# Performance work log

Measured on AMD Instinct MI355X. Metric: run time of the kernel, lower is better.

## Reference

```python
import jax, jax.numpy as jnp
import numpy as np

EPS = 1e-8
NUM_ITERATIONS = 3


def layer_norm(x, g, b, eps=EPS):
    m = jnp.mean(x, axis=-1, keepdims=True)
    v = jnp.mean((x - m) ** 2, axis=-1, keepdims=True)
    return (x - m) * jax.lax.rsqrt(v + eps) * g + b


def gru_cell(x, h, w_ih, w_hh, b_ih, b_hh):
    # PyTorch GRUCell: gates ordered (r, z, n)
    gi = x @ w_ih.T + b_ih  # [B*S, 3D]
    gh = h @ w_hh.T + b_hh
    i_r, i_z, i_n = jnp.split(gi, 3, axis=-1)
    h_r, h_z, h_n = jnp.split(gh, 3, axis=-1)
    r = jax.nn.sigmoid(i_r + h_r)
    z = jax.nn.sigmoid(i_z + h_z)
    n = jnp.tanh(i_n + r * h_n)
    return (1.0 - z) * n + z * h


def setup_inputs() -> dict:
    key = jax.random.key(0)
    ks = jax.random.split(key, 12)
    B, N, D, S = 64, 1024, 512, 16
    s = 1.0 / np.sqrt(D)
    return {
        "inputs": jax.random.normal(ks[0], (B, N, D), jnp.float32),
        "noise": jax.random.normal(ks[1], (B, S, D), jnp.float32),
        "slot_mu": jax.random.normal(ks[2], (1, 1, D), jnp.float32),
        "slot_log_sigma": jnp.zeros((1, 1, D), jnp.float32),
        "ln_in_g": jnp.ones((D,), jnp.float32),
        "ln_in_b": jnp.zeros((D,), jnp.float32),
        "ln_slots_g": jnp.ones((D,), jnp.float32),
        "ln_slots_b": jnp.zeros((D,), jnp.float32),
        "ln_mlp_g": jnp.ones((D,), jnp.float32),
        "ln_mlp_b": jnp.zeros((D,), jnp.float32),
        "Wq": jax.random.normal(ks[3], (D, D), jnp.float32) * s,
        "Wk": jax.random.normal(ks[4], (D, D), jnp.float32) * s,
        "Wv": jax.random.normal(ks[5], (D, D), jnp.float32) * s,
        "gru_w_ih": jax.random.normal(ks[6], (3 * D, D), jnp.float32) * s,
        "gru_w_hh": jax.random.normal(ks[7], (3 * D, D), jnp.float32) * s,
        "gru_b_ih": jnp.zeros((3 * D,), jnp.float32),
        "gru_b_hh": jnp.zeros((3 * D,), jnp.float32),
        "mlp_w1": jax.random.normal(ks[8], (D, D), jnp.float32) * s,
        "mlp_b1": jnp.zeros((D,), jnp.float32),
        "mlp_w2": jax.random.normal(ks[9], (D, D), jnp.float32) * s,
        "mlp_b2": jnp.zeros((D,), jnp.float32),
    }


def reference(inputs, noise, slot_mu, slot_log_sigma,
              ln_in_g, ln_in_b, ln_slots_g, ln_slots_b, ln_mlp_g, ln_mlp_b,
              Wq, Wk, Wv, gru_w_ih, gru_w_hh, gru_b_ih, gru_b_hh,
              mlp_w1, mlp_b1, mlp_w2, mlp_b2):
    B, N, D = inputs.shape
    S = noise.shape[1]
    scale = D ** (-0.5)

    # slot init: mu + sigma * eps
    slots = slot_mu + jnp.exp(slot_log_sigma) * noise  # [B,S,D]

    x = layer_norm(inputs, ln_in_g, ln_in_b)
    k = x @ Wk.T  # [B,N,D]
    v = x @ Wv.T

    for _ in range(NUM_ITERATIONS):
        slots_prev = slots
        sn = layer_norm(slots, ln_slots_g, ln_slots_b)
        q = sn @ Wq.T  # [B,S,D]
        attn_logits = jnp.einsum("bnd,bmd->bnm", q, k) * scale  # [B,S,N]
        attn = jax.nn.softmax(attn_logits, axis=-1)
        attn = attn / (jnp.sum(attn, axis=1, keepdims=True) + EPS)  # column-normalize over slots
        updates = jnp.einsum("bnm,bmd->bnd", attn, v)  # [B,S,D]
        slots = gru_cell(updates.reshape(-1, D), slots_prev.reshape(-1, D),
                         gru_w_ih, gru_w_hh, gru_b_ih, gru_b_hh).reshape(B, S, D)
        h = jax.nn.relu(layer_norm(slots, ln_mlp_g, ln_mlp_b) @ mlp_w1.T + mlp_b1)
        slots = slots + h @ mlp_w2.T + mlp_b2

    # proj_to_hidden is Identity (slot_dim == hidden_size); forward_dtype=float32
    return slots
```

## Files before the change

kernel.cpp:

```cpp
#include <hip/hip_runtime.h>
#include <hip/hip_bf16.h>
#include <cstdint>
#include <cstddef>


typedef __bf16 bf16x8 __attribute__((ext_vector_type(8)));
typedef float f32x4 __attribute__((ext_vector_type(4)));

__device__ __forceinline__ float bf2f(unsigned int u) {
  union { unsigned int i; float f; } v; v.i = u << 16; return v.f;
}
__device__ __forceinline__ unsigned short f2bf(float x) {
  __hip_bfloat16 h = __float2bfloat16(x);
  unsigned short u;
  __builtin_memcpy(&u, &h, 2);
  return u;
}

#define GLD16(gp, lp)                                                       \
  __builtin_amdgcn_global_load_lds(                                         \
      (const __attribute__((address_space(1))) void*)(gp),                  \
      (__attribute__((address_space(3))) void*)(lp), 16, 0, 0)


__global__ void wprep_k(const float* __restrict__ w1, const float* __restrict__ w2,
                        const float* __restrict__ wih, const float* __restrict__ whh,
                        const float* __restrict__ bih, const float* __restrict__ bhh,
                        const float* __restrict__ mu, const float* __restrict__ ls,
                        const float* __restrict__ noise,
                        unsigned short* __restrict__ w1_bf, unsigned short* __restrict__ w2_bf,
                        unsigned short* __restrict__ wih_bf, unsigned short* __restrict__ wcat,
                        float* __restrict__ bcat, float* __restrict__ slots) {
  int blk = blockIdx.x, t = threadIdx.x;
  if (blk < 1024) {
    int i = blk * 256 + t; w1_bf[i] = f2bf(w1[i]);
  } else if (blk < 2048) {
    int i = (blk - 1024) * 256 + t; w2_bf[i] = f2bf(w2[i]);
  } else if (blk < 5120) {
    int i = (blk - 2048) * 256 + t; wih_bf[i] = f2bf(wih[i]);
  } else if (blk < 7168) {
    int i = (blk - 5120) * 256 + t;
    int j = i >> 9, d = i & 511;
    wcat[(size_t)j * 1024 + 512 + d] = f2bf(whh[(size_t)j * 512 + d]);
  } else if (blk < 8192) {
    int i = (blk - 7168) * 256 + t;
    int j = i >> 9, d = i & 511;
    wcat[(size_t)(1536 + j) * 1024 + 512 + d] = f2bf(whh[(size_t)(1024 + j) * 512 + d]);
  } else if (blk < 10240) {
    int i = (blk - 8192) * 256 + t;
    if (i < 262144) {
      int j = i >> 9, d = i & 511;
      wcat[(size_t)(1536 + j) * 1024 + d] = 0;
    } else {
      int k = i - 262144;
      int j = k >> 9, d = k & 511;
      wcat[(size_t)(1024 + j) * 1024 + 512 + d] = 0;
    }
  } else if (blk < 10248) {
    int j = (blk - 10240) * 256 + t;
    float v;
    if (j < 1024)      v = bih[j] + bhh[j];
    else if (j < 1536) v = bih[j];
    else               v = bhh[j - 512];
    bcat[j] = v;
  } else {
    int i = (blk - 10248) * 256 + t;
    int d = i & 511;
    slots[i] = mu[d] + expf(ls[d]) * noise[i];
  }
}

__global__ __launch_bounds__(256) void tcast3_k(const float* __restrict__ Wq,
                                                const float* __restrict__ Wk,
                                                const float* __restrict__ Wv,
                                                unsigned short* __restrict__ wqT,
                                                unsigned short* __restrict__ wkT,
                                                unsigned short* __restrict__ wvT) {
  __shared__ float tt[32][33];
  const float* in = blockIdx.z == 0 ? Wq : (blockIdx.z == 1 ? Wk : Wv);
  unsigned short* out = blockIdx.z == 0 ? wqT : (blockIdx.z == 1 ? wkT : wvT);
  int c0 = blockIdx.x << 5, r0 = blockIdx.y << 5;
  int tx = threadIdx.x & 31, ty = threadIdx.x >> 5;
  #pragma unroll
  for (int i = 0; i < 4; ++i)
    tt[ty + 8 * i][tx] = in[(size_t)(r0 + ty + 8 * i) * 512 + c0 + tx];
  __syncthreads();
  #pragma unroll
  for (int i = 0; i < 4; ++i)
    out[(size_t)(c0 + ty + 8 * i) * 512 + r0 + tx] = f2bf(tt[tx][ty + 8 * i]);
}


__global__ __launch_bounds__(256) void ln_rows_k(
    const float* __restrict__ in, const float* __restrict__ g, const float* __restrict__ b,
    unsigned short* __restrict__ out, int rows) {
  int w = threadIdx.x >> 6, lane = threadIdx.x & 63;
  int row = (blockIdx.x << 2) + w;
  if (row >= rows) return;
  const float4* rp = reinterpret_cast<const float4*>(in + (size_t)row * 512);
  float4 v0 = rp[lane], v1 = rp[lane + 64];
  float s = v0.x + v0.y + v0.z + v0.w + v1.x + v1.y + v1.z + v1.w;
  float q = v0.x*v0.x + v0.y*v0.y + v0.z*v0.z + v0.w*v0.w
          + v1.x*v1.x + v1.y*v1.y + v1.z*v1.z + v1.w*v1.w;
  #pragma unroll
  for (int o = 32; o > 0; o >>= 1) { s += __shfl_xor(s, o); q += __shfl_xor(q, o); }
  float m = s * (1.0f / 512.0f);
  float rstd = rsqrtf(q * (1.0f / 512.0f) - m * m + 1e-8f);
  const float4* gp = reinterpret_cast<const float4*>(g);
  const float4* bp = reinterpret_cast<const float4*>(b);
  float4 g0 = gp[lane], g1 = gp[lane + 64];
  float4 b0 = bp[lane], b1 = bp[lane + 64];
  ushort4 o0, o1;
  o0.x = f2bf((v0.x - m) * rstd * g0.x + b0.x);
  o0.y = f2bf((v0.y - m) * rstd * g0.y + b0.y);
  o0.z = f2bf((v0.z - m) * rstd * g0.z + b0.z);
  o0.w = f2bf((v0.w - m) * rstd * g0.w + b0.w);
  o1.x = f2bf((v1.x - m) * rstd * g1.x + b1.x);
  o1.y = f2bf((v1.y - m) * rstd * g1.y + b1.y);
  o1.z = f2bf((v1.z - m) * rstd * g1.z + b1.z);
  o1.w = f2bf((v1.w - m) * rstd * g1.w + b1.w);
  ushort4* op = reinterpret_cast<ushort4*>(out + (size_t)row * 512);
  op[lane] = o0; op[lane + 64] = o1;
}


__global__ __launch_bounds__(256) void xt_k(const unsigned short* __restrict__ x,
                                            unsigned short* __restrict__ xT) {
  __shared__ unsigned short t[64][68];
  int nt = blockIdx.x, et = blockIdx.y, b = blockIdx.z;
  int r = threadIdx.x >> 3, c8 = (threadIdx.x & 7) << 3;
  #pragma unroll
  for (int p = 0; p < 2; ++p) {
    int row = r + (p << 5);
    *reinterpret_cast<uint4*>(&t[row][c8]) = *reinterpret_cast<const uint4*>(
        x + ((size_t)(b << 10) + (nt << 6) + row) * 512 + (et << 6) + c8);
  }
  __syncthreads();
  #pragma unroll
  for (int p = 0; p < 2; ++p) {
    int erow = r + (p << 5);
    ushort4 a, bb;
    #pragma unroll
    for (int j = 0; j < 4; ++j) ((unsigned short*)&a)[j] = t[c8 + j][erow];
    #pragma unroll
    for (int j = 0; j < 4; ++j) ((unsigned short*)&bb)[j] = t[c8 + 4 + j][erow];
    unsigned short* o = xT + ((size_t)(b << 9) + (et << 6) + erow) * 1024 + (nt << 6) + c8;
    *reinterpret_cast<ushort4*>(o) = a;
    *reinterpret_cast<ushort4*>(o + 4) = bb;
  }
}

__global__ __launch_bounds__(256) void gru_ln_k(
    const float* __restrict__ gates, const float* __restrict__ hp,
    const float* __restrict__ g, const float* __restrict__ b,
    float* __restrict__ sgru, unsigned short* __restrict__ lnm) {
  int w = threadIdx.x >> 6, lane = threadIdx.x & 63;
  int row = (blockIdx.x << 2) + w;
  size_t gb = (size_t)row * 2048 + (lane << 3);
  size_t hb = (size_t)row * 512 + (lane << 3);
  float rs[8], zs[8], in_[8], hn[8], hv[8], y[8];
  #pragma unroll
  for (int c = 0; c < 2; ++c) {
    *reinterpret_cast<float4*>(rs + 4*c)  = *reinterpret_cast<const float4*>(gates + gb + 4*c);
    *reinterpret_cast<float4*>(zs + 4*c)  = *reinterpret_cast<const float4*>(gates + gb + 512 + 4*c);
    *reinterpret_cast<float4*>(in_ + 4*c) = *reinterpret_cast<const float4*>(gates + gb + 1024 + 4*c);
    *reinterpret_cast<float4*>(hn + 4*c)  = *reinterpret_cast<const float4*>(gates + gb + 1536 + 4*c);
    *reinterpret_cast<float4*>(hv + 4*c)  = *reinterpret_cast<const float4*>(hp + hb + 4*c);
  }
  float s = 0.f, q = 0.f;
  #pragma unroll
  for (int j = 0; j < 8; ++j) {
    float r = 1.0f / (1.0f + expf(-rs[j]));
    float z = 1.0f / (1.0f + expf(-zs[j]));
    float n = tanhf(in_[j] + r * hn[j]);
    float h = (1.0f - z) * n + z * hv[j];
    y[j] = h; s += h; q += h * h;
  }
  #pragma unroll
  for (int o = 32; o > 0; o >>= 1) { s += __shfl_xor(s, o); q += __shfl_xor(q, o); }
  float m = s * (1.0f / 512.0f);
  float rstd = rsqrtf(q * (1.0f / 512.0f) - m * m + 1e-8f);
  const float* gg = g + (lane << 3);
  const float* bb = b + (lane << 3);
  #pragma unroll
  for (int c = 0; c < 2; ++c)
    *reinterpret_cast<float4*>(sgru + hb + 4*c) = *reinterpret_cast<const float4*>(y + 4*c);
  uint4 o4;
  unsigned int p[8];
  #pragma unroll
  for (int j = 0; j < 8; ++j) p[j] = f2bf((y[j] - m) * rstd * gg[j] + bb[j]);
  o4.x = p[0] | (p[1] << 16); o4.y = p[2] | (p[3] << 16);
  o4.z = p[4] | (p[5] << 16); o4.w = p[6] | (p[7] << 16);
  *reinterpret_cast<uint4*>(lnm + hb) = o4;
}


__global__ __launch_bounds__(256) void gemm_cat(
    const unsigned short* __restrict__ A, const unsigned short* __restrict__ W,
    unsigned short* __restrict__ Cout, int M, int N, int K, int ldc) {
  __shared__ unsigned short sA[2][8192];
  __shared__ unsigned short sB[2][8192];
  const int tid = threadIdx.x;
  const int lane = tid & 63, w = tid >> 6;

  int nwg = gridDim.x * gridDim.y;
  int flat = blockIdx.y * gridDim.x + blockIdx.x;
  if ((nwg & 7) == 0) { int c = nwg >> 3; flat = (flat & 7) * c + (flat >> 3); }
  const int row0 = (flat / gridDim.x) << 7;
  const int col0 = (flat % gridDim.x) << 7;

  const int wm = (w >> 1) << 6, wn = (w & 1) << 6;
  const int lrow = lane & 15, kt = (lane >> 4) << 3;
  const int sr8 = lane >> 3, sc8 = (lane & 7) << 3;

  f32x4 acc[4][4];
  #pragma unroll
  for (int m = 0; m < 4; ++m)
    #pragma unroll
    for (int n = 0; n < 4; ++n) acc[m][n] = f32x4{0.f, 0.f, 0.f, 0.f};

  auto stage = [&](int buf, int k0) {
    #pragma unroll
    for (int i = 0; i < 4; ++i) {
      int ii = (w << 2) + i;
      int r = (ii << 3) + sr8;
      GLD16(A + (size_t)(row0 + r) * K + k0 + sc8, &sA[buf][ii * 512]);
      GLD16(W + (size_t)(col0 + r) * K + k0 + sc8, &sB[buf][ii * 512]);
    }
  };

  stage(0, 0);
  const int nt = K >> 6;
  int cur = 0;
  for (int t = 0; t < nt; ++t) {
    __syncthreads();
    if (t + 1 < nt) stage(cur ^ 1, (t + 1) << 6);
    #pragma unroll
    for (int kk = 0; kk < 2; ++kk) {
      bf16x8 af[4], bfv[4];
      #pragma unroll
      for (int m = 0; m < 4; ++m)
        af[m] = *reinterpret_cast<const bf16x8*>(&sA[cur][(wm + m * 16 + lrow) * 64 + (kk << 5) + kt]);
      #pragma unroll
      for (int n = 0; n < 4; ++n)
        bfv[n] = *reinterpret_cast<const bf16x8*>(&sB[cur][(wn + n * 16 + lrow) * 64 + (kk << 5) + kt]);
      #pragma unroll
      for (int m = 0; m < 4; ++m)
        #pragma unroll
        for (int n = 0; n < 4; ++n)
          acc[m][n] = __builtin_amdgcn_mfma_f32_16x16x32_bf16(af[m], bfv[n], acc[m][n], 0, 0, 0);
    }
    cur ^= 1;
  }

  const int rb = (lane >> 4) << 2;
  #pragma unroll
  for (int m = 0; m < 4; ++m) {
    #pragma unroll
    for (int n = 0; n < 4; ++n) {
      int col = col0 + wn + n * 16 + lrow;
      #pragma unroll
      for (int r = 0; r < 4; ++r) {
        int row = row0 + wm + m * 16 + rb + r;
        Cout[(size_t)row * ldc + col] = f2bf(acc[m][n][r]);
      }
    }
  }
}


__global__ __launch_bounds__(256) void q2ln_k(
    const float* __restrict__ slots, const float* __restrict__ g, const float* __restrict__ b,
    const unsigned short* __restrict__ wpt, unsigned short* __restrict__ q2,
    unsigned short* __restrict__ A2) {
  __shared__ unsigned short s_sn[16 * 520];
  __shared__ unsigned short sB[2][8192];
  const int b_ = blockIdx.y, ct = blockIdx.x;
  const int lane = threadIdx.x & 63, w = threadIdx.x >> 6;
  const int lrow = lane & 15, kt = (lane >> 4) << 3;
  const int sr8 = lane >> 3, sc8 = (lane & 7) << 3;

  const float4* gp = reinterpret_cast<const float4*>(g);
  const float4* bp = reinterpret_cast<const float4*>(b);
  float4 g0 = gp[lane], g1 = gp[lane + 64];
  float4 b0 = bp[lane], b1 = bp[lane + 64];
  #pragma unroll
  for (int rr = 0; rr < 4; ++rr) {
    int r = w * 4 + rr;
    const float4* rp = reinterpret_cast<const float4*>(slots + (size_t)(b_ * 16 + r) * 512);
    float4 v0 = rp[lane], v1 = rp[lane + 64];
    float s = v0.x + v0.y + v0.z + v0.w + v1.x + v1.y + v1.z + v1.w;
    float q = v0.x*v0.x + v0.y*v0.y + v0.z*v0.z + v0.w*v0.w
            + v1.x*v1.x + v1.y*v1.y + v1.z*v1.z + v1.w*v1.w;
    #pragma unroll
    for (int o = 32; o > 0; o >>= 1) { s += __shfl_xor(s, o); q += __shfl_xor(q, o); }
    float m = s * (1.0f / 512.0f);
    float rstd = rsqrtf(q * (1.0f / 512.0f) - m * m + 1e-8f);
    ushort4 o0, o1;
    o0.x = f2bf((v0.x - m) * rstd * g0.x + b0.x);
    o0.y = f2bf((v0.y - m) * rstd * g0.y + b0.y);
    o0.z = f2bf((v0.z - m) * rstd * g0.z + b0.z);
    o0.w = f2bf((v0.w - m) * rstd * g0.w + b0.w);
    o1.x = f2bf((v1.x - m) * rstd * g1.x + b1.x);
    o1.y = f2bf((v1.y - m) * rstd * g1.y + b1.y);
    o1.z = f2bf((v1.z - m) * rstd * g1.z + b1.z);
    o1.w = f2bf((v1.w - m) * rstd * g1.w + b1.w);
    *reinterpret_cast<ushort4*>(&s_sn[r * 520 + lane * 4]) = o0;
    *reinterpret_cast<ushort4*>(&s_sn[r * 520 + 256 + lane * 4]) = o1;
    if (ct == 0) {
      ushort4 c0, c1;
      c0.x = f2bf(v0.x); c0.y = f2bf(v0.y); c0.z = f2bf(v0.z); c0.w = f2bf(v0.w);
      c1.x = f2bf(v1.x); c1.y = f2bf(v1.y); c1.z = f2bf(v1.z); c1.w = f2bf(v1.w);
      unsigned short* a2r = A2 + (size_t)(b_ * 16 + r) * 1024 + 512;
      *reinterpret_cast<ushort4*>(a2r + lane * 4) = c0;
      *reinterpret_cast<ushort4*>(a2r + 256 + lane * 4) = c1;
    }
  }

  const unsigned short* Bb = wpt + (size_t)(ct << 7) * 512;
  auto stage = [&](int buf, int k0) {
    #pragma unroll
    for (int i = 0; i < 4; ++i) {
      int ii = (w << 2) + i;
      GLD16(Bb + (size_t)((ii << 3) + sr8) * 512 + k0 + sc8, &sB[buf][ii * 512]);
    }
  };

  f32x4 acc[2];
  acc[0] = f32x4{0.f, 0.f, 0.f, 0.f};
  acc[1] = f32x4{0.f, 0.f, 0.f, 0.f};

  stage(0, 0);
  int cur = 0;
  for (int t = 0; t < 8; ++t) {
    __syncthreads();
    if (t + 1 < 8) stage(cur ^ 1, (t + 1) << 6);
    #pragma unroll
    for (int kk = 0; kk < 2; ++kk) {
      bf16x8 af = *reinterpret_cast<const bf16x8*>(&s_sn[lrow * 520 + (t << 6) + (kk << 5) + kt]);
      #pragma unroll
      for (int ni = 0; ni < 2; ++ni) {
        bf16x8 bfv = *reinterpret_cast<const bf16x8*>(
            &sB[cur][((w * 2 + ni) * 16 + lrow) * 64 + (kk << 5) + kt]);
        acc[ni] = __builtin_amdgcn_mfma_f32_16x16x32_bf16(af, bfv, acc[ni], 0, 0, 0);
      }
    }
    cur ^= 1;
  }

  const int rb = (lane >> 4) << 2;
  #pragma unroll
  for (int ni = 0; ni < 2; ++ni) {
    int col = (ct << 7) + (w * 2 + ni) * 16 + lrow;
    #pragma unroll
    for (int r = 0; r < 4; ++r) {
      int s = rb + r;
      q2[(size_t)((b_ << 4) + s) * 512 + col] = f2bf(acc[ni][r]);
    }
  }
}


__global__ __launch_bounds__(256) void logits_k(
    const unsigned short* __restrict__ q2, const unsigned short* __restrict__ x,
    unsigned short* __restrict__ out) {
  __shared__ unsigned short sA[2][1024];
  __shared__ unsigned short sB[2][8192];
  const int b = blockIdx.y, nt = blockIdx.x;
  const int lane = threadIdx.x & 63, w = threadIdx.x >> 6;
  const int lrow = lane & 15, kt = (lane >> 4) << 3;
  const int sr8 = lane >> 3, sc8 = (lane & 7) << 3;
  const unsigned short* Ab = q2 + ((size_t)b << 13);
  const unsigned short* Bb = x + (((size_t)(b << 10) + (nt << 7)) << 9);

  f32x4 acc[2];
  acc[0] = f32x4{0.f, 0.f, 0.f, 0.f};
  acc[1] = f32x4{0.f, 0.f, 0.f, 0.f};

  auto stage = [&](int buf, int k0) {
    #pragma unroll
    for (int i = 0; i < 4; ++i) {
      int ii = (w << 2) + i;
      GLD16(Bb + (size_t)((ii << 3) + sr8) * 512 + k0 + sc8, &sB[buf][ii * 512]);
    }
    if (w == 0) {
      #pragma unroll
      for (int i = 0; i < 2; ++i)
        GLD16(Ab + (size_t)((i << 3) + sr8) * 512 + k0 + sc8, &sA[buf][i * 512]);
    }
  };

  stage(0, 0);
  int cur = 0;
  for (int t = 0; t < 8; ++t) {
    __syncthreads();
    if (t + 1 < 8) stage(cur ^ 1, (t + 1) << 6);
    #pragma unroll
    for (int kk = 0; kk < 2; ++kk) {
      bf16x8 af = *reinterpret_cast<const bf16x8*>(&sA[cur][lrow * 64 + (kk << 5) + kt]);
      #pragma unroll
      for (int ni = 0; ni < 2; ++ni) {
        bf16x8 bfv = *reinterpret_cast<const bf16x8*>(
            &sB[cur][((w * 2 + ni) * 16 + lrow) * 64 + (kk << 5) + kt]);
        acc[ni] = __builtin_amdgcn_mfma_f32_16x16x32_bf16(af, bfv, acc[ni], 0, 0, 0);
      }
    }
    cur ^= 1;
  }

  const int rb = (lane >> 4) << 2;
  #pragma unroll
  for (int ni = 0; ni < 2; ++ni) {
    int n = (nt << 7) + (w * 2 + ni) * 16 + lrow;
    #pragma unroll
    for (int r = 0; r < 4; ++r) {
      int s = rb + r;
      out[(size_t)((b << 4) + s) * 1024 + n] = f2bf(acc[ni][r]);
    }
  }
}


__global__ __launch_bounds__(256) void pv_sm_k(
    const unsigned short* __restrict__ logits, const unsigned short* __restrict__ xT,
    unsigned short* __restrict__ A2) {
  __shared__ float s_mi[16][2];
  __shared__ unsigned short s_at[16 * 1032];
  __shared__ unsigned short sA[2][8192];
  const int b_ = blockIdx.y, et = blockIdx.x;
  const int lane = threadIdx.x & 63, w = threadIdx.x >> 6;
  const int lrow = lane & 15, kt = (lane >> 4) << 3;
  const int sr8 = lane >> 3, sc8 = (lane & 7) << 3;
  const unsigned short* lg = logits + ((size_t)b_ << 14);

  #pragma unroll
  for (int rr = 0; rr < 4; ++rr) {
    int r = w * 4 + rr;
    const unsigned short* rp = lg + (size_t)r * 1024;
    float v[16];
    float mx = -3.4e38f;
    #pragma unroll
    for (int i = 0; i < 16; ++i) { v[i] = bf2f(rp[lane + (i << 6)]); mx = fmaxf(mx, v[i]); }
    #pragma unroll
    for (int o = 32; o > 0; o >>= 1) mx = fmaxf(mx, __shfl_xor(mx, o));
    float s = 0.f;
    #pragma unroll
    for (int i = 0; i < 16; ++i) s += __expf(v[i] - mx);
    #pragma unroll
    for (int o = 32; o > 0; o >>= 1) s += __shfl_xor(s, o);
    if (lane == 0) { s_mi[r][0] = mx; s_mi[r][1] = 1.0f / s; }
  }
  __syncthreads();

  #pragma unroll
  for (int j = 0; j < 4; ++j) {
    int c = threadIdx.x + (j << 8);
    float e[16];
    float cs = 0.f;
    #pragma unroll
    for (int s = 0; s < 16; ++s) {
      e[s] = __expf(bf2f(lg[(size_t)s * 1024 + c]) - s_mi[s][0]) * s_mi[s][1];
      cs += e[s];
    }
    float rv = 1.0f / (cs + 1e-8f);
    #pragma unroll
    for (int s = 0; s < 16; ++s) s_at[s * 1032 + c] = f2bf(e[s] * rv);
  }

  const unsigned short* Ab = xT + ((size_t)b_ << 19) + (size_t)(et << 7) * 1024;
  auto stage = [&](int buf, int k0) {
    #pragma unroll
    for (int i = 0; i < 4; ++i) {
      int ii = (w << 2) + i;
      GLD16(Ab + (size_t)((ii << 3) + sr8) * 1024 + k0 + sc8, &sA[buf][ii * 512]);
    }
  };

  f32x4 acc[2];
  acc[0] = f32x4{0.f, 0.f, 0.f, 0.f};
  acc[1] = f32x4{0.f, 0.f, 0.f, 0.f};

  stage(0, 0);
  int cur = 0;
  for (int t = 0; t < 16; ++t) {
    __syncthreads();
    if (t + 1 < 16) stage(cur ^ 1, (t + 1) << 6);
    #pragma unroll
    for (int kk = 0; kk < 2; ++kk) {
      bf16x8 bfv = *reinterpret_cast<const bf16x8*>(&s_at[lrow * 1032 + (t << 6) + (kk << 5) + kt]);
      #pragma unroll
      for (int mi = 0; mi < 2; ++mi) {
        bf16x8 af = *reinterpret_cast<const bf16x8*>(
            &sA[cur][((w * 2 + mi) * 16 + lrow) * 64 + (kk << 5) + kt]);
        acc[mi] = __builtin_amdgcn_mfma_f32_16x16x32_bf16(af, bfv, acc[mi], 0, 0, 0);
      }
    }
    cur ^= 1;
  }

  const int rb = (lane >> 4) << 2;
  const int s = lrow;
  #pragma unroll
  for (int mi = 0; mi < 2; ++mi) {
    int e0 = (et << 7) + (w * 2 + mi) * 16 + rb;
    ushort4 o;
    o.x = f2bf(acc[mi][0]); o.y = f2bf(acc[mi][1]);
    o.z = f2bf(acc[mi][2]); o.w = f2bf(acc[mi][3]);
    *reinterpret_cast<ushort4*>(&A2[(size_t)((b_ << 4) + s) * 1024 + e0]) = o;
  }
}


template<int BIAS, int RELU, int ADDSRC, int OUTBF16, int SCALE>
__global__ __launch_bounds__(256) void gemm_sm(
    const unsigned short* __restrict__ A, const unsigned short* __restrict__ W,
    const float* __restrict__ bias, const float* __restrict__ addsrc,
    void* __restrict__ Cout, int M, int N, int K, float scalev) {
  __shared__ unsigned short sA[2][4096];
  __shared__ unsigned short sB[2][4096];
  const int tid = threadIdx.x;
  const int lane = tid & 63, w = tid >> 6;

  int nwg = gridDim.x * gridDim.y;
  int flat = blockIdx.y * gridDim.x + blockIdx.x;
  if ((nwg & 7) == 0) { int c = nwg >> 3; flat = (flat & 7) * c + (flat >> 3); }
  const int row0 = (flat / gridDim.x) << 6;
  const int col0 = (flat % gridDim.x) << 6;

  const int lrow = lane & 15, kt = (lane >> 4) << 3;
  const int sr8 = lane >> 3, sc8 = (lane & 7) << 3;

  f32x4 acc[4];
  #pragma unroll
  for (int m = 0; m < 4; ++m) acc[m] = f32x4{0.f, 0.f, 0.f, 0.f};

  auto stage = [&](int buf, int k0) {
    #pragma unroll
    for (int i = 0; i < 2; ++i) {
      int ii = (w << 1) + i;
      int r = (ii << 3) + sr8;
      GLD16(A + (size_t)(row0 + r) * K + k0 + sc8, &sA[buf][ii * 512]);
      GLD16(W + (size_t)(col0 + r) * K + k0 + sc8, &sB[buf][ii * 512]);
    }
  };

  stage(0, 0);
  const int nt = K >> 6;
  int cur = 0;
  for (int t = 0; t < nt; ++t) {
    __syncthreads();
    if (t + 1 < nt) stage(cur ^ 1, (t + 1) << 6);
    #pragma unroll
    for (int kk = 0; kk < 2; ++kk) {
      bf16x8 bfv = *reinterpret_cast<const bf16x8*>(
          &sB[cur][((w << 4) + lrow) * 64 + (kk << 5) + kt]);
      #pragma unroll
      for (int m = 0; m < 4; ++m) {
        bf16x8 af = *reinterpret_cast<const bf16x8*>(
            &sA[cur][(m * 16 + lrow) * 64 + (kk << 5) + kt]);
        acc[m] = __builtin_amdgcn_mfma_f32_16x16x32_bf16(af, bfv, acc[m], 0, 0, 0);
      }
    }
    cur ^= 1;
  }

  const int rb = (lane >> 4) << 2;
  const int col = col0 + (w << 4) + lrow;
  float bv = BIAS ? bias[col] : 0.0f;
  #pragma unroll
  for (int m = 0; m < 4; ++m) {
    #pragma unroll
    for (int r = 0; r < 4; ++r) {
      int row = row0 + m * 16 + rb + r;
      float v = acc[m][r];
      if (SCALE) v *= scalev;
      v += bv;
      if (ADDSRC) v += addsrc[(size_t)row * N + col];
      if (RELU) v = fmaxf(v, 0.0f);
      if (OUTBF16) ((unsigned short*)Cout)[(size_t)row * N + col] = f2bf(v);
      else ((float*)Cout)[(size_t)row * N + col] = v;
    }
  }
}


extern "C" void kernel_launch(void* const* d_in, const int* in_sizes, int n_in,
                              void* d_out, int out_size, void* d_ws, size_t ws_size,
                              hipStream_t stream) {
  const float* inputs  = (const float*)d_in[0];
  const float* noise   = (const float*)d_in[1];
  const float* slot_mu = (const float*)d_in[2];
  const float* slot_ls = (const float*)d_in[3];
  const float* ln_in_g = (const float*)d_in[4];
  const float* ln_in_b = (const float*)d_in[5];
  const float* ln_s_g  = (const float*)d_in[6];
  const float* ln_s_b  = (const float*)d_in[7];
  const float* ln_m_g  = (const float*)d_in[8];
  const float* ln_m_b  = (const float*)d_in[9];
  const float* Wq   = (const float*)d_in[10];
  const float* Wk   = (const float*)d_in[11];
  const float* Wv   = (const float*)d_in[12];
  const float* w_ih = (const float*)d_in[13];
  const float* w_hh = (const float*)d_in[14];
  const float* b_ih = (const float*)d_in[15];
  const float* b_hh = (const float*)d_in[16];
  const float* w1   = (const float*)d_in[17];
  const float* b1   = (const float*)d_in[18];
  const float* w2   = (const float*)d_in[19];
  const float* b2   = (const float*)d_in[20];

  const int BN = 65536, BS = 1024;

  uintptr_t base = (uintptr_t)d_ws;
  auto alloc = [&](size_t bytes) {
    void* p = (void*)base;
    base += (bytes + 255) & ~(size_t)255;
    return p;
  };
  unsigned short* x_bf    = (unsigned short*)alloc((size_t)BN * 512 * 2);
  unsigned short* xT      = (unsigned short*)alloc((size_t)64 * 512 * 1024 * 2);
  unsigned short* wqT     = (unsigned short*)alloc(512 * 512 * 2);
  unsigned short* wkT     = (unsigned short*)alloc(512 * 512 * 2);
  unsigned short* wvT     = (unsigned short*)alloc(512 * 512 * 2);
  unsigned short* wpt     = (unsigned short*)alloc(512 * 512 * 2);
  unsigned short* wih_bf  = (unsigned short*)alloc((size_t)1536 * 512 * 2);
  unsigned short* wcat_bf = (unsigned short*)alloc((size_t)2048 * 1024 * 2);
  float*          bcat    = (float*)alloc(2048 * 4);
  unsigned short* w1_bf   = (unsigned short*)alloc(512 * 512 * 2);
  unsigned short* w2_bf   = (unsigned short*)alloc(512 * 512 * 2);
  float*          slots   = (float*)alloc((size_t)BS * 512 * 4);
  unsigned short* A2      = (unsigned short*)alloc((size_t)BS * 1024 * 2);
  unsigned short* q2_bf   = (unsigned short*)alloc((size_t)BS * 512 * 2);
  unsigned short* logits  = (unsigned short*)alloc((size_t)64 * 16 * 1024 * 2);
  float*          gates   = (float*)alloc((size_t)BS * 2048 * 4);
  float*          sgru    = (float*)alloc((size_t)BS * 512 * 4);
  unsigned short* lnm_bf  = (unsigned short*)alloc((size_t)BS * 512 * 2);
  unsigned short* h_bf    = (unsigned short*)alloc((size_t)BS * 512 * 2);
  (void)ws_size; (void)n_in; (void)in_sizes; (void)out_size;

  const float scale = 0.044194173824159216f;

  wprep_k<<<12296, 256, 0, stream>>>(w1, w2, w_ih, w_hh, b_ih, b_hh,
                                     slot_mu, slot_ls, noise,
                                     w1_bf, w2_bf, wih_bf, wcat_bf, bcat, slots);
  tcast3_k<<<dim3(16, 16, 3), 256, 0, stream>>>(Wq, Wk, Wv, wqT, wkT, wvT);
  gemm_sm<0,0,0,1,1><<<dim3(8, 8), 256, 0, stream>>>(
      wkT, wqT, nullptr, nullptr, wpt, 512, 512, 512, scale);
  gemm_cat<<<dim3(4, 12), 256, 0, stream>>>(
      wih_bf, wvT, wcat_bf, 1536, 512, 512, 1024);
  ln_rows_k<<<16384, 256, 0, stream>>>(inputs, ln_in_g, ln_in_b, x_bf, BN);
  xt_k<<<dim3(16, 8, 64), 256, 0, stream>>>(x_bf, xT);

  for (int it = 0; it < 3; ++it) {
    q2ln_k<<<dim3(4, 64), 256, 0, stream>>>(slots, ln_s_g, ln_s_b, wpt, q2_bf, A2);
    logits_k<<<dim3(8, 64), 256, 0, stream>>>(q2_bf, x_bf, logits);
    pv_sm_k<<<dim3(4, 64), 256, 0, stream>>>(logits, xT, A2);
    gemm_sm<1,0,0,0,0><<<dim3(32, 16), 256, 0, stream>>>(
        A2, wcat_bf, bcat, nullptr, gates, BS, 2048, 1024, 1.0f);
    gru_ln_k<<<256, 256, 0, stream>>>(gates, slots, ln_m_g, ln_m_b, sgru, lnm_bf);
    gemm_sm<1,1,0,1,0><<<dim3(8, 16), 256, 0, stream>>>(
        lnm_bf, w1_bf, b1, nullptr, h_bf, BS, 512, 512, 1.0f);
    float* slots_out = (it == 2) ? (float*)d_out : slots;
    gemm_sm<1,0,1,0,0><<<dim3(8, 16), 256, 0, stream>>>(
        h_bf, w2_bf, b2, sgru, slots_out, BS, 512, 512, 1.0f);
  }
}
```

Measured before the change: 331.4 us.

## Fuse GRU, MLP, residual, slot LN and query projection into one per-batch kernel

New measurement: 403.0 us. 1.22x slower.

```diff
diff --git a/kernel.cpp b/kernel.cpp
--- a/kernel.cpp
+++ b/kernel.cpp
@@ -150,50 +150,6 @@
   }
 }
 
-__global__ __launch_bounds__(256) void gru_ln_k(
-    const float* __restrict__ gates, const float* __restrict__ hp,
-    const float* __restrict__ g, const float* __restrict__ b,
-    float* __restrict__ sgru, unsigned short* __restrict__ lnm) {
-  int w = threadIdx.x >> 6, lane = threadIdx.x & 63;
-  int row = (blockIdx.x << 2) + w;
-  size_t gb = (size_t)row * 2048 + (lane << 3);
-  size_t hb = (size_t)row * 512 + (lane << 3);
-  float rs[8], zs[8], in_[8], hn[8], hv[8], y[8];
-  #pragma unroll
-  for (int c = 0; c < 2; ++c) {
-    *reinterpret_cast<float4*>(rs + 4*c)  = *reinterpret_cast<const float4*>(gates + gb + 4*c);
-    *reinterpret_cast<float4*>(zs + 4*c)  = *reinterpret_cast<const float4*>(gates + gb + 512 + 4*c);
-    *reinterpret_cast<float4*>(in_ + 4*c) = *reinterpret_cast<const float4*>(gates + gb + 1024 + 4*c);
-    *reinterpret_cast<float4*>(hn + 4*c)  = *reinterpret_cast<const float4*>(gates + gb + 1536 + 4*c);
-    *reinterpret_cast<float4*>(hv + 4*c)  = *reinterpret_cast<const float4*>(hp + hb + 4*c);
-  }
-  float s = 0.f, q = 0.f;
-  #pragma unroll
-  for (int j = 0; j < 8; ++j) {
-    float r = 1.0f / (1.0f + expf(-rs[j]));
-    float z = 1.0f / (1.0f + expf(-zs[j]));
-    float n = tanhf(in_[j] + r * hn[j]);
-    float h = (1.0f - z) * n + z * hv[j];
-    y[j] = h; s += h; q += h * h;
-  }
-  #pragma unroll
-  for (int o = 32; o > 0; o >>= 1) { s += __shfl_xor(s, o); q += __shfl_xor(q, o); }
-  float m = s * (1.0f / 512.0f);
-  float rstd = rsqrtf(q * (1.0f / 512.0f) - m * m + 1e-8f);
-  const float* gg = g + (lane << 3);
-  const float* bb = b + (lane << 3);
-  #pragma unroll
-  for (int c = 0; c < 2; ++c)
-    *reinterpret_cast<float4*>(sgru + hb + 4*c) = *reinterpret_cast<const float4*>(y + 4*c);
-  uint4 o4;
-  unsigned int p[8];
-  #pragma unroll
-  for (int j = 0; j < 8; ++j) p[j] = f2bf((y[j] - m) * rstd * gg[j] + bb[j]);
-  o4.x = p[0] | (p[1] << 16); o4.y = p[2] | (p[3] << 16);
-  o4.z = p[4] | (p[5] << 16); o4.w = p[6] | (p[7] << 16);
-  *reinterpret_cast<uint4*>(lnm + hb) = o4;
-}
-
 
 __global__ __launch_bounds__(256) void gemm_cat(
     const unsigned short* __restrict__ A, const unsigned short* __restrict__ W,
@@ -511,10 +467,10 @@
 }
 
 
-template<int BIAS, int RELU, int ADDSRC, int OUTBF16, int SCALE>
+template<int BIAS, int OUTBF16, int SCALE>
 __global__ __launch_bounds__(256) void gemm_sm(
     const unsigned short* __restrict__ A, const unsigned short* __restrict__ W,
-    const float* __restrict__ bias, const float* __restrict__ addsrc,
+    const float* __restrict__ bias,
     void* __restrict__ Cout, int M, int N, int K, float scalev) {
   __shared__ unsigned short sA[2][4096];
   __shared__ unsigned short sB[2][4096];
@@ -575,10 +531,184 @@
       float v = acc[m][r];
       if (SCALE) v *= scalev;
       v += bv;
-      if (ADDSRC) v += addsrc[(size_t)row * N + col];
-      if (RELU) v = fmaxf(v, 0.0f);
       if (OUTBF16) ((unsigned short*)Cout)[(size_t)row * N + col] = f2bf(v);
       else ((float*)Cout)[(size_t)row * N + col] = v;
+    }
+  }
+}
+
+
+template<int LAST>
+__global__ __launch_bounds__(256) void update_k(
+    const float* __restrict__ gates, float* __restrict__ slots,
+    const float* __restrict__ g_m, const float* __restrict__ b_m,
+    const float* __restrict__ b1v, const float* __restrict__ b2v,
+    const unsigned short* __restrict__ w1, const unsigned short* __restrict__ w2,
+    const float* __restrict__ g_s, const float* __restrict__ b_s,
+    const unsigned short* __restrict__ wpt,
+    unsigned short* __restrict__ q2, unsigned short* __restrict__ A2,
+    float* __restrict__ out_final) {
+  __shared__ float s_y[16][516];
+  __shared__ unsigned short s_lnm[16 * 536];
+  __shared__ unsigned short s_h[16 * 536];
+  __shared__ unsigned short s_sn[16 * 536];
+  const int b = blockIdx.x;
+  const int w = threadIdx.x >> 6, lane = threadIdx.x & 63;
+  const int lrow = lane & 15, kt = (lane >> 4) << 3;
+  const int rb = (lane >> 4) << 2;
+  const int l8 = lane << 3;
+
+  {
+    const float* gg = g_m + l8;
+    const float* bb = b_m + l8;
+    #pragma unroll
+    for (int rr = 0; rr < 4; ++rr) {
+      int r = (w << 2) + rr;
+      int row = (b << 4) + r;
+      size_t gb = (size_t)row * 2048 + l8;
+      size_t hb = (size_t)row * 512 + l8;
+      float rs[8], zs[8], in_[8], hn[8], hv[8], y[8];
+      #pragma unroll
+      for (int c = 0; c < 2; ++c) {
+        *reinterpret_cast<float4*>(rs + 4*c)  = *reinterpret_cast<const float4*>(gates + gb + 4*c);
+        *reinterpret_cast<float4*>(zs + 4*c)  = *reinterpret_cast<const float4*>(gates + gb + 512 + 4*c);
+        *reinterpret_cast<float4*>(in_ + 4*c) = *reinterpret_cast<const float4*>(gates + gb + 1024 + 4*c);
+        *reinterpret_cast<float4*>(hn + 4*c)  = *reinterpret_cast<const float4*>(gates + gb + 1536 + 4*c);
+        *reinterpret_cast<float4*>(hv + 4*c)  = *reinterpret_cast<const float4*>(slots + hb + 4*c);
+      }
+      float s = 0.f, q = 0.f;
+      #pragma unroll
+      for (int j = 0; j < 8; ++j) {
+        float rg = 1.0f / (1.0f + expf(-rs[j]));
+        float zg = 1.0f / (1.0f + expf(-zs[j]));
+        float ng = tanhf(in_[j] + rg * hn[j]);
+        float hh = (1.0f - zg) * ng + zg * hv[j];
+        y[j] = hh; s += hh; q += hh * hh;
+      }
+      #pragma unroll
+      for (int o = 32; o > 0; o >>= 1) { s += __shfl_xor(s, o); q += __shfl_xor(q, o); }
+      float m = s * (1.0f / 512.0f);
+      float rstd = rsqrtf(q * (1.0f / 512.0f) - m * m + 1e-8f);
+      *reinterpret_cast<float4*>(&s_y[r][l8])     = *reinterpret_cast<float4*>(y);
+      *reinterpret_cast<float4*>(&s_y[r][l8 + 4]) = *reinterpret_cast<float4*>(y + 4);
+      unsigned int p[8];
+      #pragma unroll
+      for (int j = 0; j < 8; ++j) p[j] = f2bf((y[j] - m) * rstd * gg[j] + bb[j]);
+      uint4 o4;
+      o4.x = p[0] | (p[1] << 16); o4.y = p[2] | (p[3] << 16);
+      o4.z = p[4] | (p[5] << 16); o4.w = p[6] | (p[7] << 16);
+      *reinterpret_cast<uint4*>(&s_lnm[r * 536 + l8]) = o4;
+    }
+  }
+  __syncthreads();
+
+  {
+    f32x4 acc[8];
+    #pragma unroll
+    for (int ni = 0; ni < 8; ++ni) acc[ni] = f32x4{0.f, 0.f, 0.f, 0.f};
+    for (int k0 = 0; k0 < 512; k0 += 32) {
+      bf16x8 af = *reinterpret_cast<const bf16x8*>(&s_lnm[lrow * 536 + k0 + kt]);
+      #pragma unroll
+      for (int ni = 0; ni < 8; ++ni) {
+        int c = (w << 7) + (ni << 4) + lrow;
+        bf16x8 bfv = *reinterpret_cast<const bf16x8*>(w1 + (size_t)c * 512 + k0 + kt);
+        acc[ni] = __builtin_amdgcn_mfma_f32_16x16x32_bf16(af, bfv, acc[ni], 0, 0, 0);
+      }
+    }
+    #pragma unroll
+    for (int ni = 0; ni < 8; ++ni) {
+      int c = (w << 7) + (ni << 4) + lrow;
+      float bv = b1v[c];
+      #pragma unroll
+      for (int r4 = 0; r4 < 4; ++r4)
+        s_h[(rb + r4) * 536 + c] = f2bf(fmaxf(acc[ni][r4] + bv, 0.0f));
+    }
+  }
+  __syncthreads();
+
+  {
+    f32x4 acc[8];
+    #pragma unroll
+    for (int ni = 0; ni < 8; ++ni) acc[ni] = f32x4{0.f, 0.f, 0.f, 0.f};
+    for (int k0 = 0; k0 < 512; k0 += 32) {
+      bf16x8 af = *reinterpret_cast<const bf16x8*>(&s_h[lrow * 536 + k0 + kt]);
+      #pragma unroll
+      for (int ni = 0; ni < 8; ++ni) {
+        int c = (w << 7) + (ni << 4) + lrow;
+        bf16x8 bfv = *reinterpret_cast<const bf16x8*>(w2 + (size_t)c * 512 + k0 + kt);
+        acc[ni] = __builtin_amdgcn_mfma_f32_16x16x32_bf16(af, bfv, acc[ni], 0, 0, 0);
+      }
+    }
+    #pragma unroll
+    for (int ni = 0; ni < 8; ++ni) {
+      int c = (w << 7) + (ni << 4) + lrow;
+      float bv = b2v[c];
+      #pragma unroll
+      for (int r4 = 0; r4 < 4; ++r4)
+        s_y[rb + r4][c] = acc[ni][r4] + bv + s_y[rb + r4][c];
+    }
+  }
+  __syncthreads();
+
+  {
+    const float* gg = g_s + l8;
+    const float* bb = b_s + l8;
+    float* outp = LAST ? out_final : slots;
+    #pragma unroll
+    for (int rr = 0; rr < 4; ++rr) {
+      int r = (w << 2) + rr;
+      int row = (b << 4) + r;
+      float v[8];
+      *reinterpret_cast<float4*>(v)     = *reinterpret_cast<const float4*>(&s_y[r][l8]);
+      *reinterpret_cast<float4*>(v + 4) = *reinterpret_cast<const float4*>(&s_y[r][l8 + 4]);
+      *reinterpret_cast<float4*>(outp + (size_t)row * 512 + l8)     = *reinterpret_cast<float4*>(v);
+      *reinterpret_cast<float4*>(outp + (size_t)row * 512 + l8 + 4) = *reinterpret_cast<float4*>(v + 4);
+      if (!LAST) {
+        float s = 0.f, q = 0.f;
+        #pragma unroll
+        for (int j = 0; j < 8; ++j) { s += v[j]; q += v[j] * v[j]; }
+        #pragma unroll
+        for (int o = 32; o > 0; o >>= 1) { s += __shfl_xor(s, o); q += __shfl_xor(q, o); }
+        float m = s * (1.0f / 512.0f);
+        float rstd = rsqrtf(q * (1.0f / 512.0f) - m * m + 1e-8f);
+        unsigned int p[8], c[8];
+        #pragma unroll
+        for (int j = 0; j < 8; ++j) {
+          p[j] = f2bf((v[j] - m) * rstd * gg[j] + bb[j]);
+          c[j] = f2bf(v[j]);
+        }
+        uint4 o4, c4;
+        o4.x = p[0] | (p[1] << 16); o4.y = p[2] | (p[3] << 16);
+        o4.z = p[4] | (p[5] << 16); o4.w = p[6] | (p[7] << 16);
+        c4.x = c[0] | (c[1] << 16); c4.y = c[2] | (c[3] << 16);
+        c4.z = c[4] | (c[5] << 16); c4.w = c[6] | (c[7] << 16);
+        *reinterpret_cast<uint4*>(&s_sn[r * 536 + l8]) = o4;
+        *reinterpret_cast<uint4*>(A2 + (size_t)row * 1024 + 512 + l8) = c4;
+      }
+    }
+  }
+  if (LAST) return;
+  __syncthreads();
+
+  {
+    f32x4 acc[8];
+    #pragma unroll
+    for (int ni = 0; ni < 8; ++ni) acc[ni] = f32x4{0.f, 0.f, 0.f, 0.f};
+    for (int k0 = 0; k0 < 512; k0 += 32) {
+      bf16x8 af = *reinterpret_cast<const bf16x8*>(&s_sn[lrow * 536 + k0 + kt]);
+      #pragma unroll
+      for (int ni = 0; ni < 8; ++ni) {
+        int c = (w << 7) + (ni << 4) + lrow;
+        bf16x8 bfv = *reinterpret_cast<const bf16x8*>(wpt + (size_t)c * 512 + k0 + kt);
+        acc[ni] = __builtin_amdgcn_mfma_f32_16x16x32_bf16(af, bfv, acc[ni], 0, 0, 0);
+      }
+    }
+    #pragma unroll
+    for (int ni = 0; ni < 8; ++ni) {
+      int c = (w << 7) + (ni << 4) + lrow;
+      #pragma unroll
+      for (int r4 = 0; r4 < 4; ++r4)
+        q2[(size_t)((b << 4) + rb + r4) * 512 + c] = f2bf(acc[ni][r4]);
     }
   }
 }
@@ -633,9 +763,6 @@
   unsigned short* q2_bf   = (unsigned short*)alloc((size_t)BS * 512 * 2);
   unsigned short* logits  = (unsigned short*)alloc((size_t)64 * 16 * 1024 * 2);
   float*          gates   = (float*)alloc((size_t)BS * 2048 * 4);
-  float*          sgru    = (float*)alloc((size_t)BS * 512 * 4);
-  unsigned short* lnm_bf  = (unsigned short*)alloc((size_t)BS * 512 * 2);
-  unsigned short* h_bf    = (unsigned short*)alloc((size_t)BS * 512 * 2);
   (void)ws_size; (void)n_in; (void)in_sizes; (void)out_size;
 
   const float scale = 0.044194173824159216f;
@@ -644,24 +771,27 @@
                                      slot_mu, slot_ls, noise,
                                      w1_bf, w2_bf, wih_bf, wcat_bf, bcat, slots);
   tcast3_k<<<dim3(16, 16, 3), 256, 0, stream>>>(Wq, Wk, Wv, wqT, wkT, wvT);
-  gemm_sm<0,0,0,1,1><<<dim3(8, 8), 256, 0, stream>>>(
-      wkT, wqT, nullptr, nullptr, wpt, 512, 512, 512, scale);
+  gemm_sm<0,1,1><<<dim3(8, 8), 256, 0, stream>>>(
+      wkT, wqT, nullptr, wpt, 512, 512, 512, scale);
   gemm_cat<<<dim3(4, 12), 256, 0, stream>>>(
       wih_bf, wvT, wcat_bf, 1536, 512, 512, 1024);
   ln_rows_k<<<16384, 256, 0, stream>>>(inputs, ln_in_g, ln_in_b, x_bf, BN);
   xt_k<<<dim3(16, 8, 64), 256, 0, stream>>>(x_bf, xT);
 
+  q2ln_k<<<dim3(4, 64), 256, 0, stream>>>(slots, ln_s_g, ln_s_b, wpt, q2_bf, A2);
+
   for (int it = 0; it < 3; ++it) {
-    q2ln_k<<<dim3(4, 64), 256, 0, stream>>>(slots, ln_s_g, ln_s_b, wpt, q2_bf, A2);
     logits_k<<<dim3(8, 64), 256, 0, stream>>>(q2_bf, x_bf, logits);
     pv_sm_k<<<dim3(4, 64), 256, 0, stream>>>(logits, xT, A2);
-    gemm_sm<1,0,0,0,0><<<dim3(32, 16), 256, 0, stream>>>(
-        A2, wcat_bf, bcat, nullptr, gates, BS, 2048, 1024, 1.0f);
-    gru_ln_k<<<256, 256, 0, stream>>>(gates, slots, ln_m_g, ln_m_b, sgru, lnm_bf);
-    gemm_sm<1,1,0,1,0><<<dim3(8, 16), 256, 0, stream>>>(
-        lnm_bf, w1_bf, b1, nullptr, h_bf, BS, 512, 512, 1.0f);
-    float* slots_out = (it == 2) ? (float*)d_out : slots;
-    gemm_sm<1,0,1,0,0><<<dim3(8, 16), 256, 0, stream>>>(
-        h_bf, w2_bf, b2, sgru, slots_out, BS, 512, 512, 1.0f);
-  }
-}
+    gemm_sm<1,0,0><<<dim3(32, 16), 256, 0, stream>>>(
+        A2, wcat_bf, bcat, gates, BS, 2048, 1024, 1.0f);
+    if (it < 2)
+      update_k<0><<<64, 256, 0, stream>>>(gates, slots, ln_m_g, ln_m_b, b1, b2,
+                                          w1_bf, w2_bf, ln_s_g, ln_s_b, wpt,
+                                          q2_bf, A2, (float*)d_out);
+    else
+      update_k<1><<<64, 256, 0, stream>>>(gates, slots, ln_m_g, ln_m_b, b1, b2,
+                                          w1_bf, w2_bf, ln_s_g, ln_s_b, wpt,
+                                          q2_bf, A2, (float*)d_out);
+  }
+}
```

## Compute partial softmax row stats in logits kernel, merge in pv kernel

Applied to the files above, without the earlier changes.

Measured after the change: 322.5 us. 2.7% less time.

```diff
diff --git a/kernel.cpp b/kernel.cpp
--- a/kernel.cpp
+++ b/kernel.cpp
@@ -363,9 +363,10 @@
 
 __global__ __launch_bounds__(256) void logits_k(
     const unsigned short* __restrict__ q2, const unsigned short* __restrict__ x,
-    unsigned short* __restrict__ out) {
+    unsigned short* __restrict__ out, float* __restrict__ lstats) {
   __shared__ unsigned short sA[2][1024];
   __shared__ unsigned short sB[2][8192];
+  __shared__ float sstat[16][4][2];
   const int b = blockIdx.y, nt = blockIdx.x;
   const int lane = threadIdx.x & 63, w = threadIdx.x >> 6;
   const int lrow = lane & 15, kt = (lane >> 4) << 3;
@@ -409,21 +410,46 @@
   }
 
   const int rb = (lane >> 4) << 2;
+  unsigned short lv[2][4];
   #pragma unroll
   for (int ni = 0; ni < 2; ++ni) {
     int n = (nt << 7) + (w * 2 + ni) * 16 + lrow;
     #pragma unroll
     for (int r = 0; r < 4; ++r) {
-      int s = rb + r;
-      out[(size_t)((b << 4) + s) * 1024 + n] = f2bf(acc[ni][r]);
-    }
+      unsigned short u = f2bf(acc[ni][r]);
+      lv[ni][r] = u;
+      out[(size_t)((b << 4) + rb + r) * 1024 + n] = u;
+    }
+  }
+  #pragma unroll
+  for (int r = 0; r < 4; ++r) {
+    float v0 = bf2f(lv[0][r]), v1 = bf2f(lv[1][r]);
+    float m = fmaxf(v0, v1);
+    #pragma unroll
+    for (int o = 1; o < 16; o <<= 1) m = fmaxf(m, __shfl_xor(m, o));
+    float l = __expf(v0 - m) + __expf(v1 - m);
+    #pragma unroll
+    for (int o = 1; o < 16; o <<= 1) l += __shfl_xor(l, o);
+    if (lrow == 0) { sstat[rb + r][w][0] = m; sstat[rb + r][w][1] = l; }
+  }
+  __syncthreads();
+  if (threadIdx.x < 16) {
+    int s = threadIdx.x;
+    float m = sstat[s][0][0];
+    #pragma unroll
+    for (int c = 1; c < 4; ++c) m = fmaxf(m, sstat[s][c][0]);
+    float l = 0.f;
+    #pragma unroll
+    for (int c = 0; c < 4; ++c) l += sstat[s][c][1] * __expf(sstat[s][c][0] - m);
+    float* lp = lstats + (((size_t)(b << 4) + s) * 8 + nt) * 2;
+    lp[0] = m; lp[1] = l;
   }
 }
 
 
 __global__ __launch_bounds__(256) void pv_sm_k(
-    const unsigned short* __restrict__ logits, const unsigned short* __restrict__ xT,
-    unsigned short* __restrict__ A2) {
+    const unsigned short* __restrict__ logits, const float* __restrict__ lstats,
+    const unsigned short* __restrict__ xT, unsigned short* __restrict__ A2) {
   __shared__ float s_mi[16][2];
   __shared__ unsigned short s_at[16 * 1032];
   __shared__ unsigned short sA[2][8192];
@@ -433,22 +459,16 @@
   const int sr8 = lane >> 3, sc8 = (lane & 7) << 3;
   const unsigned short* lg = logits + ((size_t)b_ << 14);
 
-  #pragma unroll
-  for (int rr = 0; rr < 4; ++rr) {
-    int r = w * 4 + rr;
-    const unsigned short* rp = lg + (size_t)r * 1024;
-    float v[16];
-    float mx = -3.4e38f;
-    #pragma unroll
-    for (int i = 0; i < 16; ++i) { v[i] = bf2f(rp[lane + (i << 6)]); mx = fmaxf(mx, v[i]); }
-    #pragma unroll
-    for (int o = 32; o > 0; o >>= 1) mx = fmaxf(mx, __shfl_xor(mx, o));
-    float s = 0.f;
-    #pragma unroll
-    for (int i = 0; i < 16; ++i) s += __expf(v[i] - mx);
-    #pragma unroll
-    for (int o = 32; o > 0; o >>= 1) s += __shfl_xor(s, o);
-    if (lane == 0) { s_mi[r][0] = mx; s_mi[r][1] = 1.0f / s; }
+  if (threadIdx.x < 16) {
+    int s = threadIdx.x;
+    const float* lp = lstats + (((size_t)(b_ << 4) + s) * 8) * 2;
+    float m = lp[0];
+    #pragma unroll
+    for (int c = 1; c < 8; ++c) m = fmaxf(m, lp[c * 2]);
+    float l = 0.f;
+    #pragma unroll
+    for (int c = 0; c < 8; ++c) l += lp[c * 2 + 1] * __expf(lp[c * 2] - m);
+    s_mi[s][0] = m; s_mi[s][1] = 1.0f / l;
   }
   __syncthreads();
 
@@ -632,6 +652,7 @@
   unsigned short* A2      = (unsigned short*)alloc((size_t)BS * 1024 * 2);
   unsigned short* q2_bf   = (unsigned short*)alloc((size_t)BS * 512 * 2);
   unsigned short* logits  = (unsigned short*)alloc((size_t)64 * 16 * 1024 * 2);
+  float*          lstats  = (float*)alloc((size_t)64 * 16 * 8 * 2 * 4);
   float*          gates   = (float*)alloc((size_t)BS * 2048 * 4);
   float*          sgru    = (float*)alloc((size_t)BS * 512 * 4);
   unsigned short* lnm_bf  = (unsigned short*)alloc((size_t)BS * 512 * 2);
@@ -653,8 +674,8 @@
 
   for (int it = 0; it < 3; ++it) {
     q2ln_k<<<dim3(4, 64), 256, 0, stream>>>(slots, ln_s_g, ln_s_b, wpt, q2_bf, A2);
-    logits_k<<<dim3(8, 64), 256, 0, stream>>>(q2_bf, x_bf, logits);
-    pv_sm_k<<<dim3(4, 64), 256, 0, stream>>>(logits, xT, A2);
+    logits_k<<<dim3(8, 64), 256, 0, stream>>>(q2_bf, x_bf, logits, lstats);
+    pv_sm_k<<<dim3(4, 64), 256, 0, stream>>>(logits, lstats, xT, A2);
     gemm_sm<1,0,0,0,0><<<dim3(32, 16), 256, 0, stream>>>(
         A2, wcat_bf, bcat, nullptr, gates, BS, 2048, 1024, 1.0f);
     gru_ln_k<<<256, 256, 0, stream>>>(gates, slots, ln_m_g, ln_m_b, sgru, lnm_bf);
```
